# Kernel optimization log

Measured on AMD Instinct MI355X. Metric: run time of the kernel, lower is better.

Reference implementation:

```python
import jax, jax.numpy as jnp
import numpy as np

N_NODES = 20000


def _gcn_norm(edge_index, n):
    """Add self loops and compute symmetric normalization (PyG GCNConv default)."""
    loop = jnp.arange(n, dtype=edge_index.dtype)
    src = jnp.concatenate([edge_index[0], loop])  # [E+N]
    dst = jnp.concatenate([edge_index[1], loop])  # [E+N]
    deg = jax.ops.segment_sum(jnp.ones_like(dst, dtype=jnp.float32), dst, num_segments=n)
    inv_sqrt = deg ** -0.5  # deg >= 1 thanks to self loops
    norm = inv_sqrt[src] * inv_sqrt[dst]  # [E+N]
    return src, dst, norm


def _gcn_conv(x, W, b, src, dst, norm, n):
    xw = x @ W                                   # [N, out] dense transform
    msg = xw[src] * norm[:, None]                # gather + scale  [E+N, out]
    out = jax.ops.segment_sum(msg, dst, num_segments=n)  # scatter-add
    return out + b


def setup_inputs() -> dict:
    key = jax.random.key(0)
    ks = jax.random.split(key, 6)
    n, f = N_NODES, 256
    x = jax.random.normal(ks[0], (n, f), dtype=jnp.float32)
    edge_index = jax.random.randint(ks[1], (2, 320000), 0, n, dtype=jnp.int64)
    def lin(k, fi, fo):
        return jax.random.normal(k, (fi, fo), dtype=jnp.float32) * (1.0 / np.sqrt(fi))
    return {
        "x": x,
        "edge_index": edge_index,
        "W1": lin(ks[2], 256, 1024), "b1": jnp.zeros((1024,), jnp.float32),
        "W2": lin(ks[3], 1024, 512), "b2": jnp.zeros((512,), jnp.float32),
        "W3": lin(ks[4], 512, 128), "b3": jnp.zeros((128,), jnp.float32),
        "Wc": lin(ks[5], 128, 64), "bc": jnp.zeros((64,), jnp.float32),
    }


def reference(x, edge_index, W1, b1, W2, b2, W3, b3, Wc, bc):
    n = x.shape[0]
    src, dst, norm = _gcn_norm(edge_index, n)  # same graph for all layers
    h = jax.nn.relu(_gcn_conv(x, W1, b1, src, dst, norm, n))
    h = jax.nn.relu(_gcn_conv(h, W2, b2, src, dst, norm, n))
    h = jax.nn.relu(_gcn_conv(h, W3, b3, src, dst, norm, n))
    return h @ Wc + bc  # classifier logits [N, num_classes]
```

## Files before the change

### kernel.cpp

```cpp
#include <hip/hip_runtime.h>
#include <hip/hip_fp16.h>

typedef _Float16 half8 __attribute__((ext_vector_type(8)));
typedef _Float16 half4 __attribute__((ext_vector_type(4)));
typedef float floatx4 __attribute__((ext_vector_type(4)));


__device__ __forceinline__ void gload_lds16(const _Float16* g, _Float16* l) {
    __builtin_amdgcn_global_load_lds(
        (__attribute__((address_space(1))) void*)(g),
        (__attribute__((address_space(3))) void*)(l), 16, 0, 0);
}

__global__ void init_kernel(int* __restrict__ cnt, int* __restrict__ pos, int n) {
    int i = blockIdx.x * blockDim.x + threadIdx.x;
    if (i < n) { cnt[i] = 0; pos[i] = 0; }
}

__global__ void hist_kernel(const int* __restrict__ dst, int* __restrict__ cnt, int E) {
    int e = blockIdx.x * blockDim.x + threadIdx.x;
    if (e < E) atomicAdd(&cnt[dst[e]], 1);
}

__global__ void isd_kernel(const int* __restrict__ cnt, float* __restrict__ isd, int n) {
    int i = blockIdx.x * blockDim.x + threadIdx.x;
    if (i < n) isd[i] = rsqrtf((float)(cnt[i] + 1));
}

__global__ void bsum_kernel(const int* __restrict__ cnt, int* __restrict__ bsum, int n) {
    int i = blockIdx.x * 256 + threadIdx.x;
    int v = (i < n) ? cnt[i] : 0;
#pragma unroll
    for (int o = 32; o > 0; o >>= 1) v += __shfl_down(v, o);
    __shared__ int ws[4];
    int lane = threadIdx.x & 63, w = threadIdx.x >> 6;
    if (lane == 0) ws[w] = v;
    __syncthreads();
    if (threadIdx.x == 0) bsum[blockIdx.x] = ws[0] + ws[1] + ws[2] + ws[3];
}

__global__ void bscan_kernel(int* __restrict__ bsum, int nb) {
    __shared__ int sh[256];
    int t = threadIdx.x;
    int v = (t < nb) ? bsum[t] : 0;
    sh[t] = v;
    __syncthreads();
    for (int o = 1; o < 256; o <<= 1) {
        int u = (t >= o) ? sh[t - o] : 0;
        __syncthreads();
        sh[t] += u;
        __syncthreads();
    }
    if (t < nb) bsum[t] = sh[t] - v;
}

__global__ void rowptr_kernel(const int* __restrict__ cnt, const int* __restrict__ bsum,
                              int* __restrict__ row_ptr, int n, int E) {
    __shared__ int sh[256];
    int t = threadIdx.x;
    int i = blockIdx.x * 256 + t;
    int v = (i < n) ? cnt[i] : 0;
    sh[t] = v;
    __syncthreads();
    for (int o = 1; o < 256; o <<= 1) {
        int u = (t >= o) ? sh[t - o] : 0;
        __syncthreads();
        sh[t] += u;
        __syncthreads();
    }
    if (i < n) row_ptr[i] = bsum[blockIdx.x] + sh[t] - v;
    if (blockIdx.x == 0 && t == 0) row_ptr[n] = E;
}

__global__ void place_kernel(const int* __restrict__ src, const int* __restrict__ dst,
                             const float* __restrict__ isd, const int* __restrict__ row_ptr,
                             int* __restrict__ pos, int* __restrict__ s_src,
                             float* __restrict__ s_nrm, int E) {
    int e = blockIdx.x * blockDim.x + threadIdx.x;
    if (e < E) {
        int s = src[e], d = dst[e];
        int p = row_ptr[d] + atomicAdd(&pos[d], 1);
        s_src[p] = s;
        s_nrm[p] = isd[s] * isd[d];
    }
}

__global__ void f2h_kernel(const float4* __restrict__ in, half4* __restrict__ out, int n4) {
    int i = blockIdx.x * blockDim.x + threadIdx.x;
    if (i < n4) {
        float4 v = in[i];
        half4 o = { (_Float16)v.x, (_Float16)v.y, (_Float16)v.z, (_Float16)v.w };
        out[i] = o;
    }
}

__global__ void wtrans_kernel(const float* __restrict__ W, _Float16* __restrict__ Wt,
                              int fi, int fo, int fo_pad) {
    int idx = blockIdx.x * blockDim.x + threadIdx.x;
    if (idx >= fo_pad * fi) return;
    int o = idx / fi, i = idx - o * fi;
    Wt[idx] = (o < fo) ? (_Float16)W[(size_t)i * fo + o] : (_Float16)0.f;
}

template <int LPN, bool BIASRELU>
__global__ __launch_bounds__(256)
void aggv_kernel(const half8* __restrict__ xin, half8* __restrict__ xout,
                 const int* __restrict__ row_ptr, const int* __restrict__ s_src,
                 const float* __restrict__ s_nrm, const float* __restrict__ isd,
                 const float* __restrict__ bias, int n) {
    int t = blockIdx.x * blockDim.x + threadIdx.x;
    int i = t / LPN;
    int r = t % LPN;
    if (i >= n) return;
    float w = isd[i]; w *= w;
    half8 v = xin[(size_t)i * LPN + r];
    float a0[8], a1[8], a2[8], a3[8];
#pragma unroll
    for (int j = 0; j < 8; ++j) {
        a0[j] = (float)v[j] * w;
        a1[j] = 0.f; a2[j] = 0.f; a3[j] = 0.f;
    }
    int c = row_ptr[i], end = row_ptr[i + 1];
    for (; c + 8 <= end; c += 8) {
        int s0 = s_src[c],     s1 = s_src[c + 1], s2 = s_src[c + 2], s3 = s_src[c + 3];
        int s4 = s_src[c + 4], s5 = s_src[c + 5], s6 = s_src[c + 6], s7 = s_src[c + 7];
        float n0 = s_nrm[c],     n1 = s_nrm[c + 1], n2 = s_nrm[c + 2], n3 = s_nrm[c + 3];
        float n4 = s_nrm[c + 4], n5 = s_nrm[c + 5], n6 = s_nrm[c + 6], n7 = s_nrm[c + 7];
        half8 v0 = xin[(size_t)s0 * LPN + r];
        half8 v1 = xin[(size_t)s1 * LPN + r];
        half8 v2 = xin[(size_t)s2 * LPN + r];
        half8 v3 = xin[(size_t)s3 * LPN + r];
        half8 v4 = xin[(size_t)s4 * LPN + r];
        half8 v5 = xin[(size_t)s5 * LPN + r];
        half8 v6 = xin[(size_t)s6 * LPN + r];
        half8 v7 = xin[(size_t)s7 * LPN + r];
#pragma unroll
        for (int j = 0; j < 8; ++j) {
            a0[j] = fmaf((float)v0[j], n0, a0[j]);
            a1[j] = fmaf((float)v1[j], n1, a1[j]);
            a2[j] = fmaf((float)v2[j], n2, a2[j]);
            a3[j] = fmaf((float)v3[j], n3, a3[j]);
            a0[j] = fmaf((float)v4[j], n4, a0[j]);
            a1[j] = fmaf((float)v5[j], n5, a1[j]);
            a2[j] = fmaf((float)v6[j], n6, a2[j]);
            a3[j] = fmaf((float)v7[j], n7, a3[j]);
        }
    }
    for (; c + 2 <= end; c += 2) {
        int s0 = s_src[c], s1 = s_src[c + 1];
        float n0 = s_nrm[c], n1 = s_nrm[c + 1];
        half8 v0 = xin[(size_t)s0 * LPN + r];
        half8 v1 = xin[(size_t)s1 * LPN + r];
#pragma unroll
        for (int j = 0; j < 8; ++j) {
            a0[j] = fmaf((float)v0[j], n0, a0[j]);
            a1[j] = fmaf((float)v1[j], n1, a1[j]);
        }
    }
    if (c < end) {
        int s0 = s_src[c];
        float n0 = s_nrm[c];
        half8 v0 = xin[(size_t)s0 * LPN + r];
#pragma unroll
        for (int j = 0; j < 8; ++j) a0[j] = fmaf((float)v0[j], n0, a0[j]);
    }
    half8 o;
#pragma unroll
    for (int j = 0; j < 8; ++j) {
        float s = (a0[j] + a1[j]) + (a2[j] + a3[j]);
        if (BIASRELU) s = fmaxf(s + bias[r * 8 + j], 0.f);
        o[j] = (_Float16)s;
    }
    xout[(size_t)i * LPN + r] = o;
}

template <bool BIASRELU>
__global__ __launch_bounds__(256)
void agge_kernel(const half8* __restrict__ xin, half8* __restrict__ xout,
                 const int* __restrict__ row_ptr, const int* __restrict__ s_src,
                 const float* __restrict__ s_nrm, const float* __restrict__ isd,
                 const float* __restrict__ bias, int n) {
    const int D8 = 64;
    int ch = blockIdx.x & 7;
    int wid = threadIdx.x >> 6;
    int i = (blockIdx.x >> 3) * 4 + wid;
    if (i >= n) return;
    int lane = threadIdx.x & 63;
    int e8 = lane >> 3, c8 = lane & 7;
    int col8 = ch * 8 + c8;

    float a[8];
    if (e8 == 0) {
        float w = isd[i]; w *= w;
        half8 v = xin[(size_t)i * D8 + col8];
#pragma unroll
        for (int j = 0; j < 8; ++j) a[j] = (float)v[j] * w;
    } else {
#pragma unroll
        for (int j = 0; j < 8; ++j) a[j] = 0.f;
    }

    int beg = row_ptr[i], end = row_ptr[i + 1];
    for (int c = beg + e8; c < end; c += 8) {
        int s = s_src[c];
        float nr = s_nrm[c];
        half8 v = xin[(size_t)s * D8 + col8];
#pragma unroll
        for (int j = 0; j < 8; ++j) a[j] = fmaf((float)v[j], nr, a[j]);
    }

#pragma unroll
    for (int m = 8; m < 64; m <<= 1)
#pragma unroll
        for (int j = 0; j < 8; ++j) a[j] += __shfl_xor(a[j], m);

    if (e8 == 0) {
        half8 o;
#pragma unroll
        for (int j = 0; j < 8; ++j) {
            float s = a[j];
            if (BIASRELU) s = fmaxf(s + bias[col8 * 8 + j], 0.f);
            o[j] = (_Float16)s;
        }
        xout[(size_t)i * D8 + col8] = o;
    }
}

template <bool BIAS, bool RELU, bool OUT_HALF>
__global__ __launch_bounds__(256, 4)
void hgemm_kernel(const _Float16* __restrict__ A, const _Float16* __restrict__ Bt,
                  const float* __restrict__ bias, void* __restrict__ C,
                  int M, int K, int Ncout, int ldc, int gy) {
    __shared__ _Float16 As[128 * 64];
    __shared__ _Float16 Bs[64 * 64];

    int nwg = gridDim.x;
    int orig = blockIdx.x;
    int q = nwg >> 3, r = nwg & 7;
    int xcd = orig & 7, seq = orig >> 3;
    int wgid = (xcd < r ? xcd * (q + 1) : r * (q + 1) + (xcd - r) * q) + seq;
    int bx = wgid / gy, by = wgid % gy;

    const int tid = threadIdx.x;
    const int wave = tid >> 6, lane = tid & 63;
    const int l15 = lane & 15, lk = lane >> 4;
    const int wr = wave >> 1, wc = wave & 1;
    const int bm = bx * 128, bn = by * 64;

    const int sk_swz = (((tid & 7) ^ ((tid >> 3) & 7)) << 3);
    const _Float16* aSrc = A + (size_t)(bm + (tid >> 3)) * K + sk_swz;
    const _Float16* bSrc = Bt + (size_t)(bn + (tid >> 3)) * K + sk_swz;

    const int rowA = wr * 64 + l15;
    const int rowB = wc * 32 + l15;
    const int xorK = (l15 & 7) << 3;

    floatx4 acc[4][2] = {};

    const int nt = K >> 6;
    for (int t = 0; t < nt; ++t) {
        int k0 = t << 6;
#pragma unroll
        for (int i = 0; i < 4; ++i)
            gload_lds16(aSrc + k0 + (size_t)i * 32 * K, As + (i * 256 + tid) * 8);
#pragma unroll
        for (int i = 0; i < 2; ++i)
            gload_lds16(bSrc + k0 + (size_t)i * 32 * K, Bs + (i * 256 + tid) * 8);
        __syncthreads();
#pragma unroll
        for (int ks = 0; ks < 2; ++ks) {
            const int kidx = ((lk << 3) + (ks << 5)) ^ xorK;
            half8 af[4], bf[2];
#pragma unroll
            for (int mi = 0; mi < 4; ++mi)
                af[mi] = *(const half8*)(&As[(rowA + mi * 16) * 64 + kidx]);
#pragma unroll
            for (int ni = 0; ni < 2; ++ni)
                bf[ni] = *(const half8*)(&Bs[(rowB + ni * 16) * 64 + kidx]);
#pragma unroll
            for (int mi = 0; mi < 4; ++mi)
#pragma unroll
                for (int ni = 0; ni < 2; ++ni)
                    acc[mi][ni] = __builtin_amdgcn_mfma_f32_16x16x32_f16(
                        af[mi], bf[ni], acc[mi][ni], 0, 0, 0);
        }
        __syncthreads();
    }

#pragma unroll
    for (int mi = 0; mi < 4; ++mi) {
#pragma unroll
        for (int ni = 0; ni < 2; ++ni) {
            int col = bn + wc * 32 + ni * 16 + l15;
            int row0 = bm + wr * 64 + mi * 16 + lk * 4;
            floatx4 vv = acc[mi][ni];
            if (BIAS) {
                float bb = (col < Ncout) ? bias[col] : 0.f;
                vv[0] += bb; vv[1] += bb; vv[2] += bb; vv[3] += bb;
            }
            if (RELU) {
                vv[0] = fmaxf(vv[0], 0.f); vv[1] = fmaxf(vv[1], 0.f);
                vv[2] = fmaxf(vv[2], 0.f); vv[3] = fmaxf(vv[3], 0.f);
            }
            if (col < Ncout) {
#pragma unroll
                for (int rr = 0; rr < 4; ++rr) {
                    int row = row0 + rr;
                    if (row < M) {
                        if (OUT_HALF)
                            ((__half*)C)[(size_t)row * ldc + col] = __float2half(vv[rr]);
                        else
                            ((float*)C)[(size_t)row * ldc + col] = vv[rr];
                    }
                }
            }
        }
    }
}

extern "C" void kernel_launch(void* const* d_in, const int* in_sizes, int n_in,
                              void* d_out, int out_size, void* d_ws, size_t ws_size,
                              hipStream_t stream) {
    const float* x  = (const float*)d_in[0];
    const int*   ei = (const int*)d_in[1];
    const float* W1 = (const float*)d_in[2];
    const float* b1 = (const float*)d_in[3];
    const float* W2 = (const float*)d_in[4];
    const float* b2 = (const float*)d_in[5];
    const float* W3 = (const float*)d_in[6];
    const float* b3 = (const float*)d_in[7];
    const float* Wc = (const float*)d_in[8];
    const float* bc = (const float*)d_in[9];
    float* out = (float*)d_out;

    const int n = in_sizes[0] / 256;
    const int E = in_sizes[1] / 2;
    const int* src = ei;
    const int* dst = ei + E;
    const int Mpad = ((n + 127) / 128) * 128;
    const int gx = Mpad / 128;
    const int nb = (n + 255) / 256;

    size_t off = 0;
    auto take = [&](size_t bytes) -> void* {
        void* p = (char*)d_ws + off;
        off += (bytes + 255) & ~(size_t)255;
        return p;
    };
    float* isd     = (float*)take((size_t)n * 4);
    int*   cnt     = (int*)take((size_t)n * 4);
    int*   pos     = (int*)take((size_t)n * 4);
    int*   row_ptr = (int*)take((size_t)(n + 1) * 4);
    int*   bsum    = (int*)take((size_t)256 * 4);
    int*   s_src   = (int*)take((size_t)E * 4);
    float* s_nrm   = (float*)take((size_t)E * 4);
    _Float16* xh   = (_Float16*)take((size_t)n * 256 * 2);
    _Float16* a1h  = (_Float16*)take((size_t)Mpad * 256 * 2);
    _Float16* h1h  = (_Float16*)take((size_t)Mpad * 1024 * 2);
    _Float16* g2h  = (_Float16*)take((size_t)Mpad * 512 * 2);
    _Float16* a2h  = (_Float16*)take((size_t)Mpad * 512 * 2);
    _Float16* g3h  = (_Float16*)take((size_t)Mpad * 128 * 2);
    _Float16* a3h  = (_Float16*)take((size_t)Mpad * 128 * 2);
    _Float16* w1t  = (_Float16*)take((size_t)1024 * 256 * 2);
    _Float16* w2t  = (_Float16*)take((size_t)512 * 1024 * 2);
    _Float16* w3t  = (_Float16*)take((size_t)128 * 512 * 2);
    _Float16* wct  = (_Float16*)take((size_t)64 * 128 * 2);

    init_kernel<<<(n + 255) / 256, 256, 0, stream>>>(cnt, pos, n);
    hist_kernel<<<(E + 255) / 256, 256, 0, stream>>>(dst, cnt, E);
    isd_kernel<<<(n + 255) / 256, 256, 0, stream>>>(cnt, isd, n);
    bsum_kernel<<<nb, 256, 0, stream>>>(cnt, bsum, n);
    bscan_kernel<<<1, 256, 0, stream>>>(bsum, nb);
    rowptr_kernel<<<nb, 256, 0, stream>>>(cnt, bsum, row_ptr, n, E);
    place_kernel<<<(E + 255) / 256, 256, 0, stream>>>(src, dst, isd, row_ptr, pos,
                                                      s_src, s_nrm, E);

    int n4 = n * 256 / 4;
    f2h_kernel<<<(n4 + 255) / 256, 256, 0, stream>>>((const float4*)x, (half4*)xh, n4);
    wtrans_kernel<<<(1024 * 256 + 255) / 256, 256, 0, stream>>>(W1, w1t, 256, 1024, 1024);
    wtrans_kernel<<<(512 * 1024 + 255) / 256, 256, 0, stream>>>(W2, w2t, 1024, 512, 512);
    wtrans_kernel<<<(128 * 512 + 255) / 256, 256, 0, stream>>>(W3, w3t, 512, 128, 128);
    wtrans_kernel<<<(64 * 128 + 255) / 256, 256, 0, stream>>>(Wc, wct, 128, 64, 64);

    aggv_kernel<32, false><<<(n * 32 + 255) / 256, 256, 0, stream>>>(
        (const half8*)xh, (half8*)a1h, row_ptr, s_src, s_nrm, isd, nullptr, n);
    hgemm_kernel<true, true, true><<<gx * 16, 256, 0, stream>>>(
        a1h, w1t, b1, h1h, n, 256, 1024, 1024, 16);

    hgemm_kernel<false, false, true><<<gx * 8, 256, 0, stream>>>(
        h1h, w2t, nullptr, g2h, n, 1024, 512, 512, 8);
    {
        int nblk = ((n + 3) / 4) * 8;
        agge_kernel<true><<<nblk, 256, 0, stream>>>(
            (const half8*)g2h, (half8*)a2h, row_ptr, s_src, s_nrm, isd, b2, n);
    }

    hgemm_kernel<false, false, true><<<gx * 2, 256, 0, stream>>>(
        a2h, w3t, nullptr, g3h, n, 512, 128, 128, 2);
    aggv_kernel<16, true><<<(n * 16 + 255) / 256, 256, 0, stream>>>(
        (const half8*)g3h, (half8*)a3h, row_ptr, s_src, s_nrm, isd, b3, n);

    hgemm_kernel<true, false, false><<<gx * 1, 256, 0, stream>>>(
        a3h, wct, bc, out, n, 128, 64, 64, 1);
}
```

Before: 244.0 us.

## Rework aggregation thread mapping and fuse small preprocessing kernels

Replaces the per-node edge-split aggregation kernel with a templated one where a wavefront handles one node and splits its edges across ES lane groups, with four-way unrolled gathers and two accumulators. Layer 1 and layer 3 aggregations now use this wave-per-node kernel, and layer 2 switches to the vectorized lane-per-chunk kernel with 64 lanes per node. It also fuses the isd computation into the block-sum kernel and merges the four weight transpose launches into one, to cut launch overhead. The change trades occupancy and load balance across nodes of uneven degree for more memory-level parallelism in the gathers.

```diff
diff --git a/kernel.cpp b/kernel.cpp
--- a/kernel.cpp
+++ b/kernel.cpp
@@ -22,14 +22,14 @@
     if (e < E) atomicAdd(&cnt[dst[e]], 1);
 }
 
-__global__ void isd_kernel(const int* __restrict__ cnt, float* __restrict__ isd, int n) {
-    int i = blockIdx.x * blockDim.x + threadIdx.x;
-    if (i < n) isd[i] = rsqrtf((float)(cnt[i] + 1));
-}
-
-__global__ void bsum_kernel(const int* __restrict__ cnt, int* __restrict__ bsum, int n) {
+__global__ void bsum_isd_kernel(const int* __restrict__ cnt, int* __restrict__ bsum,
+                                float* __restrict__ isd, int n) {
     int i = blockIdx.x * 256 + threadIdx.x;
-    int v = (i < n) ? cnt[i] : 0;
+    int v = 0;
+    if (i < n) {
+        v = cnt[i];
+        isd[i] = rsqrtf((float)(v + 1));
+    }
 #pragma unroll
     for (int o = 32; o > 0; o >>= 1) v += __shfl_down(v, o);
     __shared__ int ws[4];
@@ -94,12 +94,33 @@
     }
 }
 
-__global__ void wtrans_kernel(const float* __restrict__ W, _Float16* __restrict__ Wt,
-                              int fi, int fo, int fo_pad) {
-    int idx = blockIdx.x * blockDim.x + threadIdx.x;
-    if (idx >= fo_pad * fi) return;
-    int o = idx / fi, i = idx - o * fi;
-    Wt[idx] = (o < fo) ? (_Float16)W[(size_t)i * fo + o] : (_Float16)0.f;
+__global__ void wtrans_all_kernel(const float* __restrict__ W1, const float* __restrict__ W2,
+                                  const float* __restrict__ W3, const float* __restrict__ Wc,
+                                  _Float16* __restrict__ w1t, _Float16* __restrict__ w2t,
+                                  _Float16* __restrict__ w3t, _Float16* __restrict__ wct) {
+    int idx = blockIdx.x * 256 + threadIdx.x;
+    if (idx < 262144) {
+        int o = idx >> 8, i2 = idx & 255;
+        w1t[idx] = (_Float16)W1[(size_t)i2 * 1024 + o];
+        return;
+    }
+    idx -= 262144;
+    if (idx < 524288) {
+        int o = idx >> 10, i2 = idx & 1023;
+        w2t[idx] = (_Float16)W2[(size_t)i2 * 512 + o];
+        return;
+    }
+    idx -= 524288;
+    if (idx < 65536) {
+        int o = idx >> 9, i2 = idx & 511;
+        w3t[idx] = (_Float16)W3[(size_t)i2 * 128 + o];
+        return;
+    }
+    idx -= 65536;
+    if (idx < 8192) {
+        int o = idx >> 7, i2 = idx & 127;
+        wct[idx] = (_Float16)Wc[(size_t)i2 * 64 + o];
+    }
 }
 
 template <int LPN, bool BIASRELU>
@@ -174,55 +195,73 @@
     xout[(size_t)i * LPN + r] = o;
 }
 
-template <bool BIASRELU>
+template <int ES, bool BIASRELU>
 __global__ __launch_bounds__(256)
-void agge_kernel(const half8* __restrict__ xin, half8* __restrict__ xout,
+void aggw_kernel(const half8* __restrict__ xin, half8* __restrict__ xout,
                  const int* __restrict__ row_ptr, const int* __restrict__ s_src,
                  const float* __restrict__ s_nrm, const float* __restrict__ isd,
                  const float* __restrict__ bias, int n) {
-    const int D8 = 64;
-    int ch = blockIdx.x & 7;
-    int wid = threadIdx.x >> 6;
-    int i = (blockIdx.x >> 3) * 4 + wid;
+    const int C8 = 64 / ES;
+    int i = blockIdx.x * 4 + (threadIdx.x >> 6);
     if (i >= n) return;
     int lane = threadIdx.x & 63;
-    int e8 = lane >> 3, c8 = lane & 7;
-    int col8 = ch * 8 + c8;
-
-    float a[8];
-    if (e8 == 0) {
+    int c8 = lane % C8;
+    int es = lane / C8;
+    float a0[8], a1[8];
+    if (es == 0) {
         float w = isd[i]; w *= w;
-        half8 v = xin[(size_t)i * D8 + col8];
-#pragma unroll
-        for (int j = 0; j < 8; ++j) a[j] = (float)v[j] * w;
+        half8 v = xin[(size_t)i * C8 + c8];
+#pragma unroll
+        for (int j = 0; j < 8; ++j) { a0[j] = (float)v[j] * w; a1[j] = 0.f; }
     } else {
 #pragma unroll
-        for (int j = 0; j < 8; ++j) a[j] = 0.f;
-    }
-
-    int beg = row_ptr[i], end = row_ptr[i + 1];
-    for (int c = beg + e8; c < end; c += 8) {
-        int s = s_src[c];
-        float nr = s_nrm[c];
-        half8 v = xin[(size_t)s * D8 + col8];
-#pragma unroll
-        for (int j = 0; j < 8; ++j) a[j] = fmaf((float)v[j], nr, a[j]);
-    }
-
-#pragma unroll
-    for (int m = 8; m < 64; m <<= 1)
-#pragma unroll
-        for (int j = 0; j < 8; ++j) a[j] += __shfl_xor(a[j], m);
-
-    if (e8 == 0) {
+        for (int j = 0; j < 8; ++j) { a0[j] = 0.f; a1[j] = 0.f; }
+    }
+    int end = row_ptr[i + 1];
+    int c = row_ptr[i] + es;
+    for (; c + 3 * ES < end; c += 4 * ES) {
+        int s0 = s_src[c];
+        int s1 = s_src[c + ES];
+        int s2 = s_src[c + 2 * ES];
+        int s3 = s_src[c + 3 * ES];
+        float n0 = s_nrm[c];
+        float n1 = s_nrm[c + ES];
+        float n2 = s_nrm[c + 2 * ES];
+        float n3 = s_nrm[c + 3 * ES];
+        half8 v0 = xin[(size_t)s0 * C8 + c8];
+        half8 v1 = xin[(size_t)s1 * C8 + c8];
+        half8 v2 = xin[(size_t)s2 * C8 + c8];
+        half8 v3 = xin[(size_t)s3 * C8 + c8];
+#pragma unroll
+        for (int j = 0; j < 8; ++j) {
+            a0[j] = fmaf((float)v0[j], n0, a0[j]);
+            a1[j] = fmaf((float)v1[j], n1, a1[j]);
+            a0[j] = fmaf((float)v2[j], n2, a0[j]);
+            a1[j] = fmaf((float)v3[j], n3, a1[j]);
+        }
+    }
+    for (; c < end; c += ES) {
+        int s0 = s_src[c];
+        float n0 = s_nrm[c];
+        half8 v0 = xin[(size_t)s0 * C8 + c8];
+#pragma unroll
+        for (int j = 0; j < 8; ++j) a0[j] = fmaf((float)v0[j], n0, a0[j]);
+    }
+#pragma unroll
+    for (int j = 0; j < 8; ++j) a0[j] += a1[j];
+#pragma unroll
+    for (int m = C8; m < 64; m <<= 1)
+#pragma unroll
+        for (int j = 0; j < 8; ++j) a0[j] += __shfl_xor(a0[j], m);
+    if (es == 0) {
         half8 o;
 #pragma unroll
         for (int j = 0; j < 8; ++j) {
-            float s = a[j];
-            if (BIASRELU) s = fmaxf(s + bias[col8 * 8 + j], 0.f);
+            float s = a0[j];
+            if (BIASRELU) s = fmaxf(s + bias[c8 * 8 + j], 0.f);
             o[j] = (_Float16)s;
         }
-        xout[(size_t)i * D8 + col8] = o;
+        xout[(size_t)i * C8 + c8] = o;
     }
 }
 
@@ -368,8 +407,7 @@
 
     init_kernel<<<(n + 255) / 256, 256, 0, stream>>>(cnt, pos, n);
     hist_kernel<<<(E + 255) / 256, 256, 0, stream>>>(dst, cnt, E);
-    isd_kernel<<<(n + 255) / 256, 256, 0, stream>>>(cnt, isd, n);
-    bsum_kernel<<<nb, 256, 0, stream>>>(cnt, bsum, n);
+    bsum_isd_kernel<<<nb, 256, 0, stream>>>(cnt, bsum, isd, n);
     bscan_kernel<<<1, 256, 0, stream>>>(bsum, nb);
     rowptr_kernel<<<nb, 256, 0, stream>>>(cnt, bsum, row_ptr, n, E);
     place_kernel<<<(E + 255) / 256, 256, 0, stream>>>(src, dst, isd, row_ptr, pos,
@@ -377,27 +415,22 @@
 
     int n4 = n * 256 / 4;
     f2h_kernel<<<(n4 + 255) / 256, 256, 0, stream>>>((const float4*)x, (half4*)xh, n4);
-    wtrans_kernel<<<(1024 * 256 + 255) / 256, 256, 0, stream>>>(W1, w1t, 256, 1024, 1024);
-    wtrans_kernel<<<(512 * 1024 + 255) / 256, 256, 0, stream>>>(W2, w2t, 1024, 512, 512);
-    wtrans_kernel<<<(128 * 512 + 255) / 256, 256, 0, stream>>>(W3, w3t, 512, 128, 128);
-    wtrans_kernel<<<(64 * 128 + 255) / 256, 256, 0, stream>>>(Wc, wct, 128, 64, 64);
-
-    aggv_kernel<32, false><<<(n * 32 + 255) / 256, 256, 0, stream>>>(
+    wtrans_all_kernel<<<(860160 + 255) / 256, 256, 0, stream>>>(
+        W1, W2, W3, Wc, w1t, w2t, w3t, wct);
+
+    aggw_kernel<2, false><<<(n + 3) / 4, 256, 0, stream>>>(
         (const half8*)xh, (half8*)a1h, row_ptr, s_src, s_nrm, isd, nullptr, n);
     hgemm_kernel<true, true, true><<<gx * 16, 256, 0, stream>>>(
         a1h, w1t, b1, h1h, n, 256, 1024, 1024, 16);
 
     hgemm_kernel<false, false, true><<<gx * 8, 256, 0, stream>>>(
         h1h, w2t, nullptr, g2h, n, 1024, 512, 512, 8);
-    {
-        int nblk = ((n + 3) / 4) * 8;
-        agge_kernel<true><<<nblk, 256, 0, stream>>>(
-            (const half8*)g2h, (half8*)a2h, row_ptr, s_src, s_nrm, isd, b2, n);
-    }
+    aggv_kernel<64, true><<<(n * 64 + 255) / 256, 256, 0, stream>>>(
+        (const half8*)g2h, (half8*)a2h, row_ptr, s_src, s_nrm, isd, b2, n);
 
     hgemm_kernel<false, false, true><<<gx * 2, 256, 0, stream>>>(
         a2h, w3t, nullptr, g3h, n, 512, 128, 128, 2);
-    aggv_kernel<16, true><<<(n * 16 + 255) / 256, 256, 0, stream>>>(
+    aggw_kernel<4, true><<<(n + 3) / 4, 256, 0, stream>>>(
         (const half8*)g3h, (half8*)a3h, row_ptr, s_src, s_nrm, isd, b3, n);
 
     hgemm_kernel<true, false, false><<<gx * 1, 256, 0, stream>>>(
```

Result: faster. 216.8 us (-11.2%).
